# Performance work log

Measured on AMD Instinct MI355X. Metric: run time of the kernel, lower is better.

The kernel has to match this reference:

```python
import jax, jax.numpy as jnp
import numpy as np


def conv2d(x, w, pad):
    # x: [N,C,H,W], w: [O,I,kh,kw]
    return jax.lax.conv_general_dilated(
        x, w, window_strides=(1, 1), padding=[(pad, pad), (pad, pad)],
        dimension_numbers=("NCHW", "OIHW", "NCHW"))


def group_norm1(x, g, b, eps=1e-5):
    # GroupNorm(1, C): normalize over (C,H,W) per sample, per-channel affine
    mu = jnp.mean(x, axis=(1, 2, 3), keepdims=True)
    var = jnp.mean((x - mu) ** 2, axis=(1, 2, 3), keepdims=True)
    xn = (x - mu) * jax.lax.rsqrt(var + eps)
    return xn * g[None, :, None, None] + b[None, :, None, None]


def maxpool_3x3_s2(x):
    return jax.lax.reduce_window(
        x, -jnp.inf, jax.lax.max, (1, 1, 3, 3), (1, 1, 2, 2),
        ((0, 0), (0, 0), (1, 1), (1, 1)))


def hr2o_layer(x, wq, wk, wv, wo, g, b):
    # x: [N,C,H,W]; pairwise attention over the N ROIs at each (h,w)
    q = conv2d(x, wq, 1)
    k = conv2d(x, wk, 1)
    v = conv2d(x, wv, 1)
    scale = 1.0 / jnp.sqrt(jnp.asarray(x.shape[1], x.dtype))
    # torch: (q.unsqueeze(1) * k.unsqueeze(0)).sum(2) == einsum over channels
    att = jnp.einsum("nchw,mchw->nmhw", q, k) * scale  # [N,N,H,W]
    att = jax.nn.softmax(att, axis=1)                    # softmax over keys (dim=1)
    virt = jnp.einsum("nmhw,mchw->nchw", att, v)        # [N,C,H,W]
    virt = jax.nn.relu(group_norm1(virt, g, b))
    virt = conv2d(virt, wo, 1)
    return x + virt  # dropout is identity in eval mode


def setup_inputs() -> dict:
    key = jax.random.key(0)
    ks = jax.random.split(key, 12)
    N, C_R, H, W, HID, NCLS, DEPTH = 64, 1024, 16, 16, 512, 60, 2
    s = 0.02
    return {
        "bg_feats": jax.random.normal(ks[0], (C_R, H, W), jnp.float32),
        "actor_feats": jax.random.normal(ks[1], (N, C_R), jnp.float32),
        "w_conv1": jax.random.normal(ks[2], (HID, 2 * C_R, 1, 1), jnp.float32) * s,
        "w_conv2": jax.random.normal(ks[3], (HID, HID, 3, 3), jnp.float32) * s,
        "w_q": jax.random.normal(ks[4], (DEPTH, HID, HID, 3, 3), jnp.float32) * s,
        "w_k": jax.random.normal(ks[5], (DEPTH, HID, HID, 3, 3), jnp.float32) * s,
        "w_v": jax.random.normal(ks[6], (DEPTH, HID, HID, 3, 3), jnp.float32) * s,
        "w_o": jax.random.normal(ks[7], (DEPTH, HID, HID, 3, 3), jnp.float32) * s,
        "gamma": jnp.ones((DEPTH, HID), jnp.float32),
        "beta": jnp.zeros((DEPTH, HID), jnp.float32),
        "w_fc1": jax.random.normal(ks[8], (HID, C_R), jnp.float32) * s,
        "w_fc2": jax.random.normal(ks[9], (NCLS, 2 * HID), jnp.float32) * s,
    }


def reference(bg_feats, actor_feats, w_conv1, w_conv2, w_q, w_k, w_v, w_o,
              gamma, beta, w_fc1, w_fc2):
    N = actor_feats.shape[0]
    C_R, H, W = bg_feats.shape
    # bg repeated per ROI, actor features tiled over spatial dims
    bg = jnp.broadcast_to(bg_feats[None], (N, C_R, H, W))
    tiled = jnp.broadcast_to(actor_feats[:, :, None, None], (N, C_R, H, W))
    x = jnp.concatenate([bg, tiled], axis=1)           # [N, 2*C_R, H, W]
    x = jax.nn.relu(conv2d(x, w_conv1, 0))             # 1x1 -> [N,HID,H,W]
    x = jax.nn.relu(conv2d(x, w_conv2, 0))             # 3x3 pad=0 -> H-2,W-2
    x = maxpool_3x3_s2(x)                              # -> 7x7
    for d in range(w_q.shape[0]):
        x = hr2o_layer(x, w_q[d], w_k[d], w_v[d], w_o[d], gamma[d], beta[d])
    high_order = jnp.mean(x, axis=(2, 3))              # gap -> [N,HID]
    roi = jax.nn.relu(actor_feats @ w_fc1.T)           # [N,HID]
    out = jnp.concatenate([roi, high_order], axis=1) @ w_fc2.T  # [N,num_classes]
    return out
```

## Files before the change

kernel.cpp:

```cpp
#include <hip/hip_runtime.h>
#include <math.h>


typedef __bf16 bf16x8 __attribute__((ext_vector_type(8)));
typedef float  f32x4  __attribute__((ext_vector_type(4)));

#define NROI 64
#define CR   1024
#define HIDC 512
#define NCLS 60
#define PLANE (NROI * HIDC * 49)
#define ROWH 40
#define OCALL 4608
#define TAPSTR ((size_t)OCALL * 512)
#define WL (HIDC * HIDC * 9)
#define GNCNT 25088.0f

#if defined(__has_builtin)
#  if __has_builtin(__builtin_amdgcn_global_load_lds)
#    define HAVE_GLL 1
#  endif
#endif

__device__ __forceinline__ void stage16(const void* g, void* lds_base, int lane) {
#ifdef HAVE_GLL
    __builtin_amdgcn_global_load_lds(
        (const __attribute__((address_space(1))) unsigned int*)g,
        (__attribute__((address_space(3))) unsigned int*)lds_base, 16, 0, 0);
#else
    *(uint4*)((char*)lds_base + lane * 16) = *(const uint4*)g;
#endif
}

__device__ __forceinline__ float bf2f(unsigned short h) {
    union { unsigned u; float f; } x; x.u = (unsigned)h << 16; return x.f;
}

__global__ __launch_bounds__(256) void k_misc(
    const float* __restrict__ w2, const float* __restrict__ wq,
    const float* __restrict__ wk, const float* __restrict__ wv,
    const float* __restrict__ wo, const float* __restrict__ bg,
    __bf16* __restrict__ wAll, __bf16* __restrict__ inT7,
    __bf16* __restrict__ bgT)
{
    const int b = blockIdx.x, tid = threadIdx.x;
    if (b < 4608) {
        const int bid = b;
        const float* src;
        if (bid < 512) src = w2 + (size_t)bid * 4608;
        else if (bid < 2048) {
            const int r = bid - 512;
            const float* bb = r < 512 ? wq : (r < 1024 ? wk : wv);
            src = bb + (size_t)(r & 511) * 4608;
        } else if (bid < 2560) src = wo + (size_t)(bid - 2048) * 4608;
        else if (bid < 4096) {
            const int r = bid - 2560;
            const float* bb = r < 512 ? wq : (r < 1024 ? wk : wv);
            src = bb + WL + (size_t)(r & 511) * 4608;
        } else src = wo + WL + (size_t)(bid - 4096) * 4608;
        __shared__ float s[4608];
        const float4* s4 = (const float4*)src;
        for (int i = tid; i < 1152; i += 256) ((float4*)s)[i] = s4[i];
        __syncthreads();
        unsigned* dst = (unsigned*)wAll;
        const int c = tid * 2;
        const int swz = ((c >> 3) & 3) ^ ((bid >> 1) & 3);
        const size_t cidx = (size_t)(c >> 5) * 32 + swz * 8 + (c & 7);
#pragma unroll
        for (int t = 0; t < 9; ++t) {
            const unsigned short u0 = __builtin_bit_cast(unsigned short, (__bf16)s[c * 9 + t]);
            const unsigned short u1 = __builtin_bit_cast(unsigned short, (__bf16)s[(c + 1) * 9 + t]);
            dst[((size_t)t * TAPSTR + (size_t)bid * 512 + cidx) / 2] =
                ((unsigned)u1 << 16) | u0;
        }
    } else if (b < 5120) {
        const int k = b - 4608;
        const int n = k >> 3;
        const int j0 = (k & 7) * 4;
#pragma unroll
        for (int i = 0; i < 4; ++i) {
            const int jj = j0 + i;
            int sp;
            if (jj < 9) sp = jj;
            else if (jj < 18) sp = 63 + jj;
            else { const int t = jj - 18; sp = (1 + (t >> 1)) * 9 + (t & 1) * 8; }
            unsigned* d = (unsigned*)(inT7 + ((size_t)n * 81 + sp) * 512);
            d[tid] = 0u;
        }
    } else {
        const int cb = (b - 5120) * 8;
        const int p = tid;
        bf16x8 v;
#pragma unroll
        for (int j = 0; j < 8; ++j)
            v[j] = (__bf16)bg[(size_t)(cb + j) * 256 + p];
        *(bf16x8*)(bgT + (size_t)p * 1024 + cb) = v;
    }
}

__global__ __launch_bounds__(256, 2) void k_ab(
    const __bf16* __restrict__ bgT, const float* __restrict__ actor,
    const float* __restrict__ w1, const float* __restrict__ wfc1,
    float* __restrict__ A_T, float* __restrict__ Bp, float* __restrict__ roi)
{
    const int bx = blockIdx.x, by = blockIdx.y;
    const bool isA = bx < 4;
    const bool isRoi = (bx == 5);
    const int ocWg = by * 64;
    const int tid = threadIdx.x;
    const int w = tid >> 6, lane = tid & 63;
    const int q = lane >> 4, l16 = lane & 15;

    __shared__ __align__(16) __bf16 s_a[64 * ROWH];
    __shared__ __align__(16) __bf16 s_b[64 * ROWH];

    f32x4 acc[4];
#pragma unroll
    for (int nt = 0; nt < 4; ++nt) acc[nt] = (f32x4){0.f, 0.f, 0.f, 0.f};

    const int row = tid >> 2, part = tid & 3;
    for (int ch = 0; ch < 32; ++ch) {
        const int c0 = ch * 32;
        __syncthreads();
        if (isA) {
            const uint4 vv = *(const uint4*)(
                bgT + (size_t)(bx * 64 + row) * 1024 + c0 + part * 8);
            *(uint4*)(&s_a[row * ROWH + part * 8]) = vv;
        } else {
            const float* src = actor + (size_t)row * CR + c0 + part * 8;
            bf16x8 val;
#pragma unroll
            for (int j = 0; j < 8; ++j) val[j] = (__bf16)src[j];
            *(bf16x8*)(&s_a[row * ROWH + part * 8]) = val;
        }
        {
            const float* srcb = isRoi
                ? (wfc1 + (size_t)(ocWg + row) * CR + c0 + part * 8)
                : (w1 + (size_t)(ocWg + row) * (2 * CR)
                      + (isA ? 0 : CR) + c0 + part * 8);
            bf16x8 vb;
#pragma unroll
            for (int j = 0; j < 8; ++j) vb[j] = (__bf16)srcb[j];
            *(bf16x8*)(&s_b[row * ROWH + part * 8]) = vb;
        }
        __syncthreads();
        const bf16x8 af = *(const bf16x8*)(&s_a[(w * 16 + l16) * ROWH + q * 8]);
#pragma unroll
        for (int nt = 0; nt < 4; ++nt) {
            const bf16x8 bw = *(const bf16x8*)(&s_b[(nt * 16 + l16) * ROWH + q * 8]);
            acc[nt] = __builtin_amdgcn_mfma_f32_16x16x32_bf16(af, bw, acc[nt], 0, 0, 0);
        }
    }
#pragma unroll
    for (int r = 0; r < 4; ++r) {
#pragma unroll
        for (int nt = 0; nt < 4; ++nt) {
            const int mrow = w * 16 + q * 4 + r;
            const int oc = ocWg + nt * 16 + l16;
            if (isA)       A_T[(size_t)(bx * 64 + mrow) * 512 + oc] = acc[nt][r];
            else if (isRoi) roi[(size_t)mrow * 512 + oc] = fmaxf(acc[nt][r], 0.f);
            else           Bp[(size_t)mrow * 512 + oc] = acc[nt][r];
        }
    }
}

__global__ __launch_bounds__(256) void k_prep_in2(
    const float* __restrict__ A_T, const float* __restrict__ B,
    __bf16* __restrict__ dst)
{
    const int vn = blockIdx.x;
    const int n = vn >> 2, quad = vn & 3;
    const int sp0 = blockIdx.y * 27;
    const float b0 = B[n * HIDC + threadIdx.x];
    const float b1 = B[n * HIDC + 256 + threadIdx.x];
    for (int sp = sp0; sp < sp0 + 27; ++sp) {
        const int r = sp / 9, w = sp % 9;
        const int p16 = ((quad >> 1) * 7 + r) * 16 + (quad & 1) * 7 + w;
        __bf16* d = dst + ((size_t)vn * 81 + sp) * 512;
        d[threadIdx.x]       = (__bf16)fmaxf(A_T[p16 * HIDC + threadIdx.x] + b0, 0.f);
        d[256 + threadIdx.x] = (__bf16)fmaxf(A_T[p16 * HIDC + 256 + threadIdx.x] + b1, 0.f);
    }
}

template<int VN, int MODE>
__global__ __launch_bounds__(256, (VN == 4) ? 2 : 3) void k_conv_pipe(
    const __bf16* __restrict__ inT,
    const __bf16* __restrict__ wAll, int ocBaseGl,
    __bf16* __restrict__ outb,
    float* __restrict__ zeroStats, float* __restrict__ gapZero)
{
    constexpr int MT = (VN == 4) ? 4 : 2;
    constexpr int SLOTS = VN * 324;
    constexpr int NSUB = (SLOTS + 255) / 256;
    constexpr int SBUF = NSUB * 256;
    const int tid = threadIdx.x;
    const int w = tid >> 6, lane = tid & 63;
    const int q = lane >> 4, l16 = lane & 15;
    const int vn_l = (VN == 4) ? w : (w & 1);
    const int mh   = (VN == 4) ? 0 : (w >> 1);
    const int vnBase = blockIdx.x * VN;
    const int ocWg = blockIdx.y * 64;

    if (zeroStats && blockIdx.x == 0 && blockIdx.y == 0 && tid < 128)
        zeroStats[tid] = 0.f;
    if (gapZero && blockIdx.y == 0 && blockIdx.x < 16) {
        const float4 z = {0.f, 0.f, 0.f, 0.f};
        ((float4*)gapZero)[blockIdx.x * 512 + tid * 2]     = z;
        ((float4*)gapZero)[blockIdx.x * 512 + tid * 2 + 1] = z;
    }

    __shared__ __align__(16) __bf16 s_w[2 * 2048];
    __shared__ __align__(16) __bf16 s_in[2 * SBUF * 8];

    unsigned iGo[NSUB];
#pragma unroll
    for (int s = 0; s < NSUB; ++s) {
        int idx = tid + s * 256;
        if (idx > SLOTS - 1) idx = SLOTS - 1;
        const int vnl = idx / 324, rem = idx - vnl * 324;
        const int r = rem >> 2, part = rem & 3;
        iGo[s] = (unsigned)(((vnBase + vnl) * 81 + r) * 512
                            + ((part ^ (r & 3)) * 8));
    }
    const unsigned wGo = (unsigned)((ocBaseGl + ocWg + (tid >> 2)) * 512
                                    + (tid & 3) * 8);
    const int bOff = l16 * 32 + ((q ^ ((l16 >> 1) & 3)) << 3);

    int aLoc[MT];
#pragma unroll
    for (int mt = 0; mt < MT; ++mt) {
        int p = (mh * MT + mt) * 16 + l16;
        p = p > 48 ? 48 : p;
        aLoc[mt] = (p / 7) * 9 + (p % 7);
    }
    const int vb81 = vn_l * 81;

    f32x4 acc[MT][4];
#pragma unroll
    for (int a = 0; a < MT; ++a)
#pragma unroll
        for (int b = 0; b < 4; ++b) acc[a][b] = (f32x4){0.f, 0.f, 0.f, 0.f};

#pragma unroll
    for (int s = 0; s < NSUB; ++s)
        stage16(inT + iGo[s],
                (char*)s_in + (size_t)(s * 256 + w * 64) * 16, lane);
    stage16(wAll + wGo, (char*)s_w + (size_t)w * 1024, lane);

    for (int ch = 0; ch < 16; ++ch) {
        const int c0 = ch * 32;
        const int chPar = ch & 1;
        const int nxt = chPar ^ 1;
#pragma unroll
        for (int t = 0; t < 9; ++t) {
            {
                const int tapN = (t + 1) % 9;
                const int cc = (t == 8) ? (c0 + 32) : c0;
                const int parN = (chPar + t + 1) & 1;
                stage16(wAll + (size_t)tapN * TAPSTR + wGo + cc,
                        (char*)s_w + (size_t)parN * 4096 + (size_t)w * 1024,
                        lane);
            }
            if (t < NSUB)
                stage16(inT + iGo[t] + c0 + 32,
                        (char*)s_in + (size_t)nxt * (SBUF * 16)
                                    + (size_t)(t * 256 + w * 64) * 16, lane);
            const int Wt = (VN == 4)
                ? ((t == 0) ? 2 : (t <= 5) ? 3 : (t == 6) ? 2 : 1)
                : ((t == 0) ? 2 : (t <= 2) ? 3 : (t == 3) ? 2 : 1);
            if (Wt == 3)      asm volatile("s_waitcnt vmcnt(3)" ::: "memory");
            else if (Wt == 2) asm volatile("s_waitcnt vmcnt(2)" ::: "memory");
            else              asm volatile("s_waitcnt vmcnt(1)" ::: "memory");
            __builtin_amdgcn_sched_barrier(0);
            __builtin_amdgcn_s_barrier();
            __builtin_amdgcn_sched_barrier(0);
            {
                const int par = (chPar + t) & 1;
                const int DT = (t / 3) * 9 + (t % 3);
                bf16x8 bw[4];
#pragma unroll
                for (int nt = 0; nt < 4; ++nt)
                    bw[nt] = *(const bf16x8*)(&s_w[par * 2048 + nt * 512 + bOff]);
                bf16x8 af[MT];
#pragma unroll
                for (int mt = 0; mt < MT; ++mt) {
                    const int rl = aLoc[mt] + DT;
                    const int col = (q ^ (rl & 3)) << 3;
                    af[mt] = *(const bf16x8*)(
                        &s_in[chPar * (SBUF * 8) + (vb81 + rl) * 32 + col]);
                }
#pragma unroll
                for (int mt = 0; mt < MT; ++mt)
#pragma unroll
                    for (int nt = 0; nt < 4; ++nt)
                        acc[mt][nt] = __builtin_amdgcn_mfma_f32_16x16x32_bf16(
                            af[mt], bw[nt], acc[mt][nt], 0, 0, 0);
            }
            __builtin_amdgcn_sched_barrier(0);
            __builtin_amdgcn_s_barrier();
        }
    }

    const int vn = vnBase + vn_l;
#pragma unroll
    for (int mt = 0; mt < MT; ++mt) {
#pragma unroll
        for (int r = 0; r < 4; ++r) {
            const int p = (mh * MT + mt) * 16 + q * 4 + r;
            if (p >= 49) continue;
#pragma unroll
            for (int nt = 0; nt < 4; ++nt) {
                const int oc = ocWg + nt * 16 + l16;
                const float v = acc[mt][nt][r];
                if (MODE == 2) {
                    const int n = vn >> 2, quad = vn & 3;
                    const int p14 = ((quad >> 1) * 7 + p / 7) * 14 + (quad & 1) * 7 + p % 7;
                    outb[((size_t)n * 196 + p14) * 512 + oc] = (__bf16)fmaxf(v, 0.f);
                } else {
                    const int conv = oc >> 9;
                    outb[(size_t)conv * PLANE + ((size_t)p * 64 + vn) * 512 + (oc & 511)]
                        = (__bf16)v;
                }
            }
        }
    }
}

template<int VN, bool GNIN>
__global__ __launch_bounds__(256, 2) void k_conv_mfma(
    const __bf16* __restrict__ inT,
    const float* __restrict__ vin,
    const float* __restrict__ statsRaw,
    const float* __restrict__ gamma, const float* __restrict__ beta,
    const __bf16* __restrict__ wAll, int ocBaseGl,
    const float* __restrict__ resid, float* __restrict__ outf,
    __bf16* __restrict__ outb, __bf16* __restrict__ inT7out,
    float* __restrict__ zeroStats, float* __restrict__ gapOut,
    float* __restrict__ gapZero, int mode)
{
    constexpr int MT = (VN == 4) ? 4 : ((VN == 2) ? 2 : 1);
    const int tid = threadIdx.x;
    const int w = tid >> 6, lane = tid & 63;
    const int q = lane >> 4, l16 = lane & 15;
    const int vn_l = (VN == 4) ? w : ((VN == 2) ? (w & 1) : 0);
    const int mh   = (VN == 4) ? 0 : ((VN == 2) ? (w >> 1) : w);
    const int vnBase = blockIdx.x * VN;
    const int ocWg = blockIdx.y * 64;

    if (zeroStats && blockIdx.x == 0 && blockIdx.y == 0 && tid < 128)
        zeroStats[tid] = 0.f;
    if (gapZero && blockIdx.y == 0 && blockIdx.x < 16) {
        const float4 z = {0.f, 0.f, 0.f, 0.f};
        ((float4*)gapZero)[blockIdx.x * 512 + tid * 2]     = z;
        ((float4*)gapZero)[blockIdx.x * 512 + tid * 2 + 1] = z;
    }

    __shared__ __align__(16) __bf16 s_w[9 * 64 * 32];
    __shared__ __align__(16) __bf16 s_in[VN * 81 * ROWH];
    __shared__ float s_mi[VN][2];
    __shared__ float s_gb[GNIN ? 1024 : 4];

    if (GNIN) {
        for (int k = tid; k < 512; k += 256) {
            s_gb[k]       = gamma[k];
            s_gb[512 + k] = beta[k];
        }
        if (tid < VN) {
            const float S = statsRaw[(vnBase + tid) * 2];
            const float Q = statsRaw[(vnBase + tid) * 2 + 1];
            const float mean = S / GNCNT;
            const float var  = Q / GNCNT - mean * mean;
            s_mi[tid][0] = mean;
            s_mi[tid][1] = rsqrtf(var + 1e-5f);
        }
    }

    const int bSwz = (q ^ ((l16 >> 1) & 3)) << 3;
    int aBase[MT];
#pragma unroll
    for (int mt = 0; mt < MT; ++mt) {
        int p = (mh * MT + mt) * 16 + l16;
        p = p > 48 ? 48 : p;
        aBase[mt] = (vn_l * 81 + (p / 7) * 9 + (p % 7)) * ROWH + q * 8;
    }

    f32x4 acc[MT][4];
#pragma unroll
    for (int a = 0; a < MT; ++a)
#pragma unroll
        for (int b = 0; b < 4; ++b) acc[a][b] = (f32x4){0.f, 0.f, 0.f, 0.f};

    for (int ch = 0; ch < 16; ++ch) {
        const int c0 = ch * 32;
        __syncthreads();
#pragma unroll
        for (int i = 0; i < 9; ++i) {
            const int s0 = (w * 9 + i) * 64;
            const int s = s0 + lane;
            const int t = s >> 8;
            const int rem = s & 255;
            const int row = rem >> 2, part = rem & 3;
            const __bf16* g = wAll + (size_t)t * TAPSTR
                + (size_t)(ocBaseGl + ocWg + row) * 512 + c0 + part * 8;
            stage16(g, (char*)s_w + (size_t)s0 * 16, lane);
        }
        for (int idx = tid; idx < VN * 324; idx += 256) {
            const int vnl = idx / 324, rem = idx - vnl * 324;
            const int r = rem >> 2, part = rem & 3;
            if (GNIN) {
                const int rr = r / 9, cc = r % 9;
                bf16x8 val;
                if (rr >= 1 && rr <= 7 && cc >= 1 && cc <= 7) {
                    const int p = (rr - 1) * 7 + (cc - 1);
                    const float* src = vin +
                        ((size_t)(vnBase + vnl) * 49 + p) * 512 + c0 + part * 8;
                    const float m = s_mi[vnl][0], iv = s_mi[vnl][1];
#pragma unroll
                    for (int j = 0; j < 8; ++j)
                        val[j] = (__bf16)fmaxf(
                            (src[j] - m) * iv * s_gb[c0 + part * 8 + j]
                            + s_gb[512 + c0 + part * 8 + j], 0.f);
                } else {
#pragma unroll
                    for (int j = 0; j < 8; ++j) val[j] = (__bf16)0.f;
                }
                *(bf16x8*)(&s_in[(vnl * 81 + r) * ROWH + part * 8]) = val;
            } else {
                const uint4 vv = *(const uint4*)(
                    inT + ((size_t)(vnBase + vnl) * 81 + r) * 512 + c0 + part * 8);
                *(uint4*)(&s_in[(vnl * 81 + r) * ROWH + part * 8]) = vv;
            }
        }
        __syncthreads();
#pragma unroll
        for (int t = 0; t < 9; ++t) {
            const int tOffA = ((t / 3) * 9 + (t % 3)) * ROWH;
            bf16x8 bw[4];
#pragma unroll
            for (int nt = 0; nt < 4; ++nt)
                bw[nt] = *(const bf16x8*)(&s_w[(t * 64 + nt * 16 + l16) * 32 + bSwz]);
            bf16x8 af[MT];
#pragma unroll
            for (int mt = 0; mt < MT; ++mt)
                af[mt] = *(const bf16x8*)(&s_in[aBase[mt] + tOffA]);
#pragma unroll
            for (int mt = 0; mt < MT; ++mt)
#pragma unroll
                for (int nt = 0; nt < 4; ++nt)
                    acc[mt][nt] = __builtin_amdgcn_mfma_f32_16x16x32_bf16(
                        af[mt], bw[nt], acc[mt][nt], 0, 0, 0);
        }
    }

    const int vn = vnBase + vn_l;
    float gsum[4] = {0.f, 0.f, 0.f, 0.f};
#pragma unroll
    for (int mt = 0; mt < MT; ++mt) {
#pragma unroll
        for (int r = 0; r < 4; ++r) {
            const int p = (mh * MT + mt) * 16 + q * 4 + r;
            if (p >= 49) continue;
#pragma unroll
            for (int nt = 0; nt < 4; ++nt) {
                const int oc = ocWg + nt * 16 + l16;
                const float v = acc[mt][nt][r];
                if (mode == 2) {
                    const int n = vn >> 2, quad = vn & 3;
                    const int p14 = ((quad >> 1) * 7 + p / 7) * 14 + (quad & 1) * 7 + p % 7;
                    outb[((size_t)n * 196 + p14) * 512 + oc] = (__bf16)fmaxf(v, 0.f);
                } else if (mode == 1) {
                    const size_t addr = ((size_t)vn * 49 + p) * 512 + oc;
                    const float res = v + resid[addr];
                    if (!gapOut) outf[addr] = res;
                    gsum[nt] += res;
                    if (inT7out) {
                        const int sp = (p / 7 + 1) * 9 + (p % 7 + 1);
                        inT7out[((size_t)vn * 81 + sp) * 512 + oc] = (__bf16)res;
                    }
                } else {
                    const int conv = oc >> 9;
                    outb[(size_t)conv * PLANE + ((size_t)p * 64 + vn) * 512 + (oc & 511)]
                        = (__bf16)v;
                }
            }
        }
    }
    if (gapOut) {
#pragma unroll
        for (int nt = 0; nt < 4; ++nt)
            atomicAdd(gapOut + (size_t)vn * 512 + ocWg + nt * 16 + l16, gsum[nt]);
    }
}

__global__ __launch_bounds__(256) void k_pool_prep(
    const __bf16* __restrict__ x2, __bf16* __restrict__ inT7,
    float* __restrict__ xA)
{
    const int b = blockIdx.x;
    const int n = b / 49, p = b % 49;
    const int i = p / 7, j = p % 7;
    const int sp = (i + 1) * 9 + (j + 1);
#pragma unroll
    for (int k = 0; k < 2; ++k) {
        const int c = threadIdx.x + k * 256;
        float mx = -1e30f;
#pragma unroll
        for (int di = -1; di <= 1; ++di) {
            const int rr = 2 * i + di;
            if (rr < 0 || rr >= 14) continue;
#pragma unroll
            for (int dj = -1; dj <= 1; ++dj) {
                const int cc = 2 * j + dj;
                if (cc < 0 || cc >= 14) continue;
                mx = fmaxf(mx, (float)x2[((size_t)n * 196 + rr * 14 + cc) * 512 + c]);
            }
        }
        inT7[((size_t)n * 81 + sp) * 512 + c] = (__bf16)mx;
        xA[((size_t)n * 49 + p) * 512 + c] = mx;
    }
}

__global__ __launch_bounds__(256) void k_attvirt(
    const __bf16* __restrict__ qT, const __bf16* __restrict__ kT,
    const __bf16* __restrict__ vT, float* __restrict__ virt,
    float* __restrict__ statsRaw)
{
    const int p = blockIdx.y;
    const int w = threadIdx.x >> 6, m = threadIdx.x & 63;
    const int n = blockIdx.x * 4 + w;
    __shared__ float s_q[4][HIDC];
    __shared__ float s_a[4][64];
    {
        const uint4 v = ((const uint4*)(qT + ((size_t)p * 64 + n) * HIDC))[m];
        const unsigned* u = (const unsigned*)&v;
#pragma unroll
        for (int j = 0; j < 4; ++j) {
            s_q[w][m * 8 + 2 * j]     = bf2f((unsigned short)(u[j] & 0xffff));
            s_q[w][m * 8 + 2 * j + 1] = bf2f((unsigned short)(u[j] >> 16));
        }
    }
    __syncthreads();
    const uint4* krow = (const uint4*)(kT + ((size_t)p * 64 + m) * HIDC);
    float acc0 = 0.f, acc1 = 0.f;
    for (int i = 0; i < 64; ++i) {
        const uint4 v = krow[i];
        const unsigned* u = (const unsigned*)&v;
#pragma unroll
        for (int j = 0; j < 2; ++j) {
            acc0 = fmaf(s_q[w][i * 8 + 2 * j],     bf2f((unsigned short)(u[j] & 0xffff)), acc0);
            acc0 = fmaf(s_q[w][i * 8 + 2 * j + 1], bf2f((unsigned short)(u[j] >> 16)),    acc0);
        }
#pragma unroll
        for (int j = 2; j < 4; ++j) {
            acc1 = fmaf(s_q[w][i * 8 + 2 * j],     bf2f((unsigned short)(u[j] & 0xffff)), acc1);
            acc1 = fmaf(s_q[w][i * 8 + 2 * j + 1], bf2f((unsigned short)(u[j] >> 16)),    acc1);
        }
    }
    float acc = (acc0 + acc1) * 0.044194173824159216f;
    float mx = acc;
#pragma unroll
    for (int off = 32; off; off >>= 1) mx = fmaxf(mx, __shfl_xor(mx, off));
    const float e = expf(acc - mx);
    float s = e;
#pragma unroll
    for (int off = 32; off; off >>= 1) s += __shfl_xor(s, off);
    s_a[w][m] = e / s;
    __syncthreads();
    const int c0 = m * 8;
    float av[8];
#pragma unroll
    for (int j = 0; j < 8; ++j) av[j] = 0.f;
    for (int mm = 0; mm < 64; ++mm) {
        const float a = s_a[w][mm];
        const uint4 v = *(const uint4*)(vT + ((size_t)p * 64 + mm) * HIDC + c0);
        const unsigned* u = (const unsigned*)&v;
#pragma unroll
        for (int j = 0; j < 4; ++j) {
            av[2 * j]     = fmaf(a, bf2f((unsigned short)(u[j] & 0xffff)), av[2 * j]);
            av[2 * j + 1] = fmaf(a, bf2f((unsigned short)(u[j] >> 16)),    av[2 * j + 1]);
        }
    }
    float* o = virt + ((size_t)n * 49 + p) * 512 + c0;
    float ps = 0.f, pq = 0.f;
#pragma unroll
    for (int j = 0; j < 8; ++j) {
        o[j] = av[j];
        ps += av[j];
        pq = fmaf(av[j], av[j], pq);
    }
#pragma unroll
    for (int off = 32; off; off >>= 1) {
        ps += __shfl_xor(ps, off);
        pq += __shfl_xor(pq, off);
    }
    if (m == 0) {
        atomicAdd(statsRaw + n * 2, ps);
        atomicAdd(statsRaw + n * 2 + 1, pq);
    }
}

__global__ __launch_bounds__(256) void k_final(
    const float* __restrict__ roi, const float* __restrict__ gap,
    const float* __restrict__ wfc2, float* __restrict__ out)
{
    const int n = blockIdx.x, tid = threadIdx.x;
    __shared__ float s[1024];
    s[tid]       = roi[(size_t)n * 512 + tid];
    s[tid + 256] = roi[(size_t)n * 512 + 256 + tid];
    s[tid + 512] = gap[(size_t)n * 512 + tid] * (1.f / 49.f);
    s[tid + 768] = gap[(size_t)n * 512 + 256 + tid] * (1.f / 49.f);
    __syncthreads();
    if (tid < 240) {
        const int k = tid >> 2, part = tid & 3;
        const float4* w4 = (const float4*)(wfc2 + (size_t)k * 1024 + part * 256);
        const float4* s4 = (const float4*)(s + part * 256);
        float a0 = 0.f, a1 = 0.f, a2 = 0.f, a3 = 0.f;
        for (int i = 0; i < 64; ++i) {
            const float4 wv = w4[i], sv = s4[i];
            a0 = fmaf(wv.x, sv.x, a0); a1 = fmaf(wv.y, sv.y, a1);
            a2 = fmaf(wv.z, sv.z, a2); a3 = fmaf(wv.w, sv.w, a3);
        }
        float acc = (a0 + a1) + (a2 + a3);
        acc += __shfl_xor(acc, 1);
        acc += __shfl_xor(acc, 2);
        if (part == 0) out[n * NCLS + k] = acc;
    }
}

extern "C" void kernel_launch(void* const* d_in, const int* in_sizes, int n_in,
                              void* d_out, int out_size, void* d_ws, size_t ws_size,
                              hipStream_t stream) {
    const float* bg    = (const float*)d_in[0];
    const float* actor = (const float*)d_in[1];
    const float* w1    = (const float*)d_in[2];
    const float* w2    = (const float*)d_in[3];
    const float* wq    = (const float*)d_in[4];
    const float* wk    = (const float*)d_in[5];
    const float* wv    = (const float*)d_in[6];
    const float* wo    = (const float*)d_in[7];
    const float* gamma = (const float*)d_in[8];
    const float* beta  = (const float*)d_in[9];
    const float* wfc1  = (const float*)d_in[10];
    const float* wfc2  = (const float*)d_in[11];
    float* out = (float*)d_out;
    float* ws  = (float*)d_ws;

    float* A_T   = ws;
    float* Bp    = A_T + 131072;
    float* xA    = Bp + 32768;
    float* xB    = xA + PLANE;
    float* stats = xB + PLANE;
    float* roi   = stats + 128;
    float* gap   = roi + 32768;
    float* fend  = gap + 32768;
    __bf16* x2h  = (__bf16*)fend;
    float*  virt = (float*)x2h;
    __bf16* inT2 = x2h + 6422528;
    __bf16* qkvT = inT2;
    __bf16* inT7 = inT2 + 10616832;
    __bf16* wAll = inT7 + 2654208;
    __bf16* bgT  = wAll + (size_t)9 * OCALL * 512;

    k_misc<<<5248, 256, 0, stream>>>(w2, wq, wk, wv, wo, bg, wAll, inT7, bgT);
    k_ab<<<dim3(6, 8), 256, 0, stream>>>(bgT, actor, w1, wfc1, A_T, Bp, roi);
    k_prep_in2<<<dim3(256, 3), 256, 0, stream>>>(A_T, Bp, inT2);
    k_conv_pipe<4, 2><<<dim3(64, 8), 256, 0, stream>>>(
        inT2, wAll, 0, x2h, nullptr, nullptr);
    k_pool_prep<<<64 * 49, 256, 0, stream>>>(x2h, inT7, xA);

    float* xin = xA;
    float* xout = xB;
    for (int d = 0; d < 2; ++d) {
        k_conv_pipe<2, 0><<<dim3(32, 24), 256, 0, stream>>>(
            inT7, wAll, 512 + d * 2048, qkvT, stats,
            d == 1 ? gap : nullptr);
        k_attvirt<<<dim3(16, 49), 256, 0, stream>>>(
            qkvT, qkvT + PLANE, qkvT + 2 * PLANE, virt, stats);
        k_conv_mfma<1, true><<<dim3(64, 8), 256, 0, stream>>>(
            nullptr, virt, stats, gamma + d * HIDC, beta + d * HIDC,
            wAll, 2048 + d * 2048, xin, xout, nullptr,
            d == 0 ? inT7 : nullptr, nullptr,
            d == 1 ? gap : nullptr, nullptr, 1);
        float* t = xin; xin = xout; xout = t;
    }
    k_final<<<64, 256, 0, stream>>>(roi, gap, wfc2, out);
}
```

Baseline: 645.1 us.

## Stage three conv taps per pipeline step to cut barriers per channel chunk

Restructures the 3x3 conv pipeline so each step stages a full row of three weight taps and a third of the input sub-tiles, then runs three taps of MFMAs between one pair of barriers instead of one tap per barrier. This cuts barrier and waitcnt overhead per 32-channel chunk from nine steps to three. In exchange the weight LDS buffer grows threefold, which may lower occupancy. The vmcnt thresholds are rewritten and assume NSUB divisible by three, which is fragile.

```diff
diff --git a/kernel.cpp b/kernel.cpp
--- a/kernel.cpp
+++ b/kernel.cpp
@@ -193,6 +193,7 @@
     constexpr int SLOTS = VN * 324;
     constexpr int NSUB = (SLOTS + 255) / 256;
     constexpr int SBUF = NSUB * 256;
+    constexpr int NI = NSUB / 3;
     const int tid = threadIdx.x;
     const int w = tid >> 6, lane = tid & 63;
     const int q = lane >> 4, l16 = lane & 15;
@@ -209,7 +210,7 @@
         ((float4*)gapZero)[blockIdx.x * 512 + tid * 2 + 1] = z;
     }
 
-    __shared__ __align__(16) __bf16 s_w[2 * 2048];
+    __shared__ __align__(16) __bf16 s_w[2 * 3 * 2048];
     __shared__ __align__(16) __bf16 s_in[2 * SBUF * 8];
 
     unsigned iGo[NSUB];
@@ -245,49 +246,61 @@
     for (int s = 0; s < NSUB; ++s)
         stage16(inT + iGo[s],
                 (char*)s_in + (size_t)(s * 256 + w * 64) * 16, lane);
-    stage16(wAll + wGo, (char*)s_w + (size_t)w * 1024, lane);
+#pragma unroll
+    for (int j = 0; j < 3; ++j)
+        stage16(wAll + (size_t)j * TAPSTR + wGo,
+                (char*)s_w + (size_t)j * 4096 + (size_t)w * 1024, lane);
+    __syncthreads();
 
     for (int ch = 0; ch < 16; ++ch) {
         const int c0 = ch * 32;
-        const int chPar = ch & 1;
-        const int nxt = chPar ^ 1;
-#pragma unroll
-        for (int t = 0; t < 9; ++t) {
+        const int cur = ch & 1;
+        const int nxt = cur ^ 1;
+#pragma unroll
+        for (int f = 0; f < 3; ++f) {
+            const int P = ch * 3 + f;
+            const int wpar = P & 1;
             {
-                const int tapN = (t + 1) % 9;
-                const int cc = (t == 8) ? (c0 + 32) : c0;
-                const int parN = (chPar + t + 1) & 1;
-                stage16(wAll + (size_t)tapN * TAPSTR + wGo + cc,
-                        (char*)s_w + (size_t)parN * 4096 + (size_t)w * 1024,
-                        lane);
+                const int fn = (f == 2) ? 0 : (f + 1);
+                const int cc = (f == 2) ? (c0 + 32) : c0;
+#pragma unroll
+                for (int j = 0; j < 3; ++j)
+                    stage16(wAll + (size_t)(fn * 3 + j) * TAPSTR + wGo + cc,
+                            (char*)s_w + (size_t)((wpar ^ 1) * 3 + j) * 4096
+                                        + (size_t)w * 1024, lane);
             }
-            if (t < NSUB)
-                stage16(inT + iGo[t] + c0 + 32,
+#pragma unroll
+            for (int u = 0; u < NI; ++u) {
+                const int s = f * NI + u;
+                stage16(inT + iGo[s] + c0 + 32,
                         (char*)s_in + (size_t)nxt * (SBUF * 16)
-                                    + (size_t)(t * 256 + w * 64) * 16, lane);
-            const int Wt = (VN == 4)
-                ? ((t == 0) ? 2 : (t <= 5) ? 3 : (t == 6) ? 2 : 1)
-                : ((t == 0) ? 2 : (t <= 2) ? 3 : (t == 3) ? 2 : 1);
-            if (Wt == 3)      asm volatile("s_waitcnt vmcnt(3)" ::: "memory");
-            else if (Wt == 2) asm volatile("s_waitcnt vmcnt(2)" ::: "memory");
-            else              asm volatile("s_waitcnt vmcnt(1)" ::: "memory");
+                                    + (size_t)(s * 256 + w * 64) * 16, lane);
+            }
+            if (f == 0) {
+                if constexpr (NI == 2) asm volatile("s_waitcnt vmcnt(5)" ::: "memory");
+                else                   asm volatile("s_waitcnt vmcnt(4)" ::: "memory");
+            } else {
+                if constexpr (NI == 2) asm volatile("s_waitcnt vmcnt(7)" ::: "memory");
+                else                   asm volatile("s_waitcnt vmcnt(5)" ::: "memory");
+            }
             __builtin_amdgcn_sched_barrier(0);
             __builtin_amdgcn_s_barrier();
             __builtin_amdgcn_sched_barrier(0);
-            {
-                const int par = (chPar + t) & 1;
-                const int DT = (t / 3) * 9 + (t % 3);
+#pragma unroll
+            for (int j = 0; j < 3; ++j) {
+                const int DT = f * 9 + j;
                 bf16x8 bw[4];
 #pragma unroll
                 for (int nt = 0; nt < 4; ++nt)
-                    bw[nt] = *(const bf16x8*)(&s_w[par * 2048 + nt * 512 + bOff]);
+                    bw[nt] = *(const bf16x8*)(
+                        &s_w[(wpar * 3 + j) * 2048 + nt * 512 + bOff]);
                 bf16x8 af[MT];
 #pragma unroll
                 for (int mt = 0; mt < MT; ++mt) {
                     const int rl = aLoc[mt] + DT;
                     const int col = (q ^ (rl & 3)) << 3;
                     af[mt] = *(const bf16x8*)(
-                        &s_in[chPar * (SBUF * 8) + (vb81 + rl) * 32 + col]);
+                        &s_in[cur * (SBUF * 8) + (vb81 + rl) * 32 + col]);
                 }
 #pragma unroll
                 for (int mt = 0; mt < MT; ++mt)
```

New measurement: 602.0 us. 1.07x faster.
